# Kernel optimization log

Measured on AMD Instinct MI355X. Metric: run time of the kernel, lower is better.

## Reference

```python
import jax, jax.numpy as jnp
import numpy as np

D_IN = 1024
D_OUT = 1024
NUM_HEADS = 16
HEAD_DIM = D_OUT // NUM_HEADS


def setup_inputs() -> dict:
    key = jax.random.key(0)
    ks = jax.random.split(key, 7)
    s = 0.02
    x = jax.random.normal(ks[0], (2, 2048, D_IN), dtype=jnp.float32)
    # torch nn.Linear stores weight as [out, in]; y = x @ W.T + b
    w_k = jax.random.normal(ks[1], (D_OUT, D_IN), dtype=jnp.float32) * s
    w_q = jax.random.normal(ks[2], (D_OUT, D_IN), dtype=jnp.float32) * s
    w_v = jax.random.normal(ks[3], (D_OUT, D_IN), dtype=jnp.float32) * s
    w_o = jax.random.normal(ks[4], (D_OUT, D_OUT), dtype=jnp.float32) * s
    b_o = jax.random.normal(ks[5], (D_OUT,), dtype=jnp.float32) * s
    return {"x": x, "w_k": w_k, "w_q": w_q, "w_v": w_v, "w_o": w_o, "b_o": b_o}


def reference(x, w_k, w_q, w_v, w_o, b_o):
    b, L, _ = x.shape
    # NOTE (faithful to source): queries are produced by k_w, keys by q_w
    q = jnp.einsum('bld,od->blo', x, w_k)  # weighted_q = k_w(x)
    k = jnp.einsum('bld,od->blo', x, w_q)  # weighted_k = q_w(x)
    v = jnp.einsum('bld,od->blo', x, w_v)
    # [b, H, L, hd]
    q = q.reshape(b, L, NUM_HEADS, HEAD_DIM).transpose(0, 2, 1, 3)
    k = k.reshape(b, L, NUM_HEADS, HEAD_DIM).transpose(0, 2, 1, 3)
    v = v.reshape(b, L, NUM_HEADS, HEAD_DIM).transpose(0, 2, 1, 3)
    scores = jnp.einsum('bhqd,bhkd->bhqk', q, k)  # [b,H,L,L]
    causal = jnp.triu(jnp.ones((L, L), dtype=bool), k=1)  # True above diagonal
    scores = jnp.where(causal[None, None], -jnp.inf, scores)
    scale = jnp.float32(1.0 / np.sqrt(D_OUT))  # source scales by 1/sqrt(d_out)
    attn = jax.nn.softmax(scores * scale, axis=-1)
    ctx = jnp.einsum('bhqk,bhkd->bhqd', attn, v)
    ctx = ctx.transpose(0, 2, 1, 3).reshape(b, L, D_OUT)
    return jnp.einsum('blo,po->blp', ctx, w_o) + b_o
```

## Files before the change

### kernel.cpp

```cpp
#include <hip/hip_runtime.h>
#include <hip/hip_bf16.h>


typedef __attribute__((ext_vector_type(8))) short bf16x8;
typedef __attribute__((ext_vector_type(4))) float f32x4;

#define SEQ 2048
#define NHEAD 16
#define HD 64
#define M_TOT 4096

static __device__ __forceinline__ unsigned short f2bf(float f) {
  unsigned int u = __float_as_uint(f);
  u += 0x7fff + ((u >> 16) & 1);
  return (unsigned short)(u >> 16);
}
static __device__ __forceinline__ float bf2f(unsigned short u) {
  return __uint_as_float(((unsigned int)u) << 16);
}
static __device__ __forceinline__ unsigned int cvt_pk_bf16(float lo, float hi) {
  unsigned int r;
  asm("v_cvt_pk_bf16_f32 %0, %1, %2" : "=v"(r) : "v"(lo), "v"(hi));
  return r;
}

static __device__ __forceinline__ void gload16(const unsigned short* g, unsigned short* l) {
  __builtin_amdgcn_global_load_lds(
      (const __attribute__((address_space(1))) unsigned int*)g,
      (__attribute__((address_space(3))) unsigned int*)l, 16, 0, 0);
}

__global__ void cvt_kernel(const float* __restrict__ in, unsigned short* __restrict__ out, int n) {
  int i = (blockIdx.x * blockDim.x + threadIdx.x) * 4;
  if (i >= n) return;
  float4 v = *reinterpret_cast<const float4*>(in + i);
  ushort4 o;
  o.x = f2bf(v.x); o.y = f2bf(v.y); o.z = f2bf(v.z); o.w = f2bf(v.w);
  *reinterpret_cast<ushort4*>(out + i) = o;
}

__global__ void cvt4_kernel(const float* __restrict__ w0, const float* __restrict__ w1,
                            const float* __restrict__ w2, const float* __restrict__ w3,
                            unsigned short* __restrict__ o0, unsigned short* __restrict__ o1,
                            unsigned short* __restrict__ o2, unsigned short* __restrict__ o3) {
  const float* in; unsigned short* out;
  switch (blockIdx.y) {
    case 0: in = w0; out = o0; break;
    case 1: in = w1; out = o1; break;
    case 2: in = w2; out = o2; break;
    default: in = w3; out = o3; break;
  }
  int i = (blockIdx.x * blockDim.x + threadIdx.x) * 4;
  float4 v = *reinterpret_cast<const float4*>(in + i);
  ushort4 o;
  o.x = f2bf(v.x); o.y = f2bf(v.y); o.z = f2bf(v.z); o.w = f2bf(v.w);
  *reinterpret_cast<ushort4*>(out + i) = o;
}

template <int BN, int MODE>
__global__ __launch_bounds__(256) void gemm_tile(
    const unsigned short* __restrict__ A,
    const unsigned short* __restrict__ B,
    int K,
    unsigned short* __restrict__ qb,
    unsigned short* __restrict__ kb,
    unsigned short* __restrict__ vtb,
    const float* __restrict__ bias,
    float* __restrict__ outf)
{
  constexpr int NFR = BN / 32;
  __shared__ unsigned short lds_a[128 * 64];
  __shared__ unsigned short lds_b[BN * 64];
  const int t = threadIdx.x;
  const int wid = t >> 6;
  const int lane = t & 63;
  const int lr = lane & 15;
  const int lg = lane >> 4;
  const int tm = blockIdx.x * 128;
  const int tn = blockIdx.y * BN;
  const int wr = (wid >> 1) * 64;
  const int wc = (wid & 1) * (BN / 2);

  const unsigned short* Ab = A + (size_t)tm * K;
  const unsigned short* Bb = B + (size_t)tn * K;
  const int srow = wid * 8 + (lane >> 3);
  const int scol = (lane & 7) * 8;

  f32x4 acc[4][NFR];
  #pragma unroll
  for (int i = 0; i < 4; ++i)
    #pragma unroll
    for (int j = 0; j < NFR; ++j) acc[i][j] = (f32x4){0.f, 0.f, 0.f, 0.f};

  for (int k0 = 0; k0 < K; k0 += 64) {
    #pragma unroll
    for (int i = 0; i < 4; ++i)
      gload16(Ab + (size_t)(i * 32 + srow) * K + k0 + scol, &lds_a[(i * 32 + wid * 8) * 64]);
    #pragma unroll
    for (int i = 0; i < NFR; ++i)
      gload16(Bb + (size_t)(i * 32 + srow) * K + k0 + scol, &lds_b[(i * 32 + wid * 8) * 64]);
    __syncthreads();
    #pragma unroll
    for (int kk = 0; kk < 2; ++kk) {
      bf16x8 af[4], bfr[NFR];
      #pragma unroll
      for (int mi = 0; mi < 4; ++mi)
        af[mi] = *reinterpret_cast<const bf16x8*>(&lds_a[(wr + mi * 16 + lr) * 64 + kk * 32 + lg * 8]);
      #pragma unroll
      for (int ni = 0; ni < NFR; ++ni)
        bfr[ni] = *reinterpret_cast<const bf16x8*>(&lds_b[(wc + ni * 16 + lr) * 64 + kk * 32 + lg * 8]);
      #pragma unroll
      for (int mi = 0; mi < 4; ++mi)
        #pragma unroll
        for (int ni = 0; ni < NFR; ++ni)
          acc[mi][ni] = __builtin_amdgcn_mfma_f32_16x16x32_bf16(af[mi], bfr[ni], acc[mi][ni], 0, 0, 0);
    }
    __syncthreads();
  }

  if (MODE == 0) {
    #pragma unroll
    for (int mi = 0; mi < 4; ++mi)
      #pragma unroll
      for (int ni = 0; ni < NFR; ++ni)
        #pragma unroll
        for (int r = 0; r < 4; ++r) {
          int gm = tm + wr + mi * 16 + lg * 4 + r;
          int gn = tn + wc + ni * 16 + lr;
          float v = acc[mi][ni][r];
          unsigned short bv = f2bf(v);
          int bb = gm >> 11, l = gm & 2047;
          int tsel = gn >> 10, o = gn & 1023;
          int h = o >> 6, d = o & 63;
          if (tsel == 0)      qb[(((size_t)(bb * NHEAD + h)) * SEQ + l) * HD + d] = bv;
          else if (tsel == 1) kb[(((size_t)(bb * NHEAD + h)) * SEQ + l) * HD + d] = bv;
          else                vtb[(((size_t)(bb * NHEAD + h)) * HD + d) * SEQ + l] = bv;
        }
  } else {
    #pragma unroll
    for (int mi = 0; mi < 4; ++mi)
      #pragma unroll
      for (int ni = 0; ni < NFR; ++ni)
        #pragma unroll
        for (int r = 0; r < 4; ++r) {
          int gm = tm + wr + mi * 16 + lg * 4 + r;
          int gn = tn + wc + ni * 16 + lr;
          outf[(size_t)gm * 1024 + gn] = acc[mi][ni][r] + bias[gn];
        }
  }
}

__global__ __launch_bounds__(256) void attn_kernel(
    const unsigned short* __restrict__ qb,
    const unsigned short* __restrict__ kb,
    const unsigned short* __restrict__ vtb,
    unsigned short* __restrict__ ctxb)
{
  __shared__ unsigned short kt_lds[2][64 * 64];
  __shared__ unsigned short vt_lds[2][64 * 64];
  __shared__ unsigned short p_lds[4][16 * 64];

  const int t = threadIdx.x;
  const int wid = t >> 6;
  const int lane = t & 63;
  const int lr = lane & 15;
  const int lg = lane >> 4;

  const int id = blockIdx.x;
  const int xcd = id & 7;
  const int chunk = id >> 3;
  const int bh = xcd * 4 + (chunk >> 4);
  const int pair = chunk & 15;
  const int b = bh >> 4, h = bh & 15;

  const float csc = (1.0f / 32.0f) * 1.44269504f;

  const unsigned short* Kp = kb + (size_t)bh * SEQ * HD;
  const unsigned short* Vp = vtb + (size_t)bh * HD * SEQ;
  const int sr_ = lane >> 3;
  const int sg_ = lane & 7;

  auto stage = [&](int buf, int kv0) {
    #pragma unroll
    for (int i = 0; i < 2; ++i) {
      int r = i * 32 + wid * 8 + sr_;
      int g = sg_ ^ (r & 7);
      gload16(Kp + (size_t)(kv0 + r) * HD + g * 8, &kt_lds[buf][(i * 32 + wid * 8) * 64]);
      gload16(Vp + (size_t)r * SEQ + kv0 + g * 8, &vt_lds[buf][(i * 32 + wid * 8) * 64]);
    }
  };

  for (int ph = 0; ph < 2; ++ph) {
    const int qtile = ph ? pair : (31 - pair);
    const int qw = qtile * 64 + wid * 16;

    const unsigned short* Qp = qb + ((size_t)bh * SEQ + qw) * HD;
    bf16x8 aq[2];
    #pragma unroll
    for (int kk = 0; kk < 2; ++kk) {
      bf16x8 raw = *reinterpret_cast<const bf16x8*>(&Qp[lr * HD + kk * 32 + lg * 8]);
      #pragma unroll
      for (int j = 0; j < 8; ++j)
        aq[kk][j] = (short)f2bf(bf2f((unsigned short)raw[j]) * csc);
    }

    f32x4 oacc[4];
    #pragma unroll
    for (int ni = 0; ni < 4; ++ni) oacc[ni] = (f32x4){0.f, 0.f, 0.f, 0.f};
    float m_ = -INFINITY, ls = 0.f;

    stage(0, 0);
    __syncthreads();
    int cur = 0;

    for (int kt = 0; kt <= qtile; ++kt) {
      const int kv0 = kt * 64;
      if (kt < qtile) stage(cur ^ 1, kv0 + 64);

      const char* kbase = (const char*)&kt_lds[cur][0];
      f32x4 s4[4];
      #pragma unroll
      for (int ni = 0; ni < 4; ++ni) {
        int row = ni * 16 + lr;
        int xr = (row & 7) << 4;
        bf16x8 b0 = *reinterpret_cast<const bf16x8*>(kbase + (row * 128 + ((lg * 16) ^ xr)));
        bf16x8 b1 = *reinterpret_cast<const bf16x8*>(kbase + (row * 128 + ((64 + lg * 16) ^ xr)));
        s4[ni] = (f32x4){0.f, 0.f, 0.f, 0.f};
        s4[ni] = __builtin_amdgcn_mfma_f32_16x16x32_bf16(b0, aq[0], s4[ni], 0, 0, 0);
        s4[ni] = __builtin_amdgcn_mfma_f32_16x16x32_bf16(b1, aq[1], s4[ni], 0, 0, 0);
      }

      if (kt == qtile) {
        #pragma unroll
        for (int ni = 0; ni < 4; ++ni)
          #pragma unroll
          for (int r = 0; r < 4; ++r)
            if (ni * 16 + lg * 4 + r > wid * 16 + lr) s4[ni][r] = -INFINITY;
      }

      float rmax;
      {
        float a0 = fmaxf(fmaxf(s4[0][0], s4[0][1]), fmaxf(s4[0][2], s4[0][3]));
        float a1 = fmaxf(fmaxf(s4[1][0], s4[1][1]), fmaxf(s4[1][2], s4[1][3]));
        float a2 = fmaxf(fmaxf(s4[2][0], s4[2][1]), fmaxf(s4[2][2], s4[2][3]));
        float a3 = fmaxf(fmaxf(s4[3][0], s4[3][1]), fmaxf(s4[3][2], s4[3][3]));
        rmax = fmaxf(fmaxf(a0, a1), fmaxf(a2, a3));
        rmax = fmaxf(rmax, __shfl_xor(rmax, 16));
        rmax = fmaxf(rmax, __shfl_xor(rmax, 32));
      }

      if (__any(rmax > m_ + 8.f)) {
        float mn = fmaxf(m_, rmax);
        float f = exp2f(m_ - mn);
        m_ = mn;
        ls *= f;
        #pragma unroll
        for (int r = 0; r < 4; ++r) {
          float fo = __shfl(f, lg * 4 + r);
          #pragma unroll
          for (int ni = 0; ni < 4; ++ni) oacc[ni][r] *= fo;
        }
      }

      float p[4][4];
      float psum = 0.f;
      #pragma unroll
      for (int ni = 0; ni < 4; ++ni) {
        float t0 = exp2f(s4[ni][0] - m_);
        float t1 = exp2f(s4[ni][1] - m_);
        float t2 = exp2f(s4[ni][2] - m_);
        float t3 = exp2f(s4[ni][3] - m_);
        p[ni][0] = t0; p[ni][1] = t1; p[ni][2] = t2; p[ni][3] = t3;
        psum += (t0 + t1) + (t2 + t3);
      }
      psum += __shfl_xor(psum, 16);
      psum += __shfl_xor(psum, 32);
      ls += psum;

      char* pbase = (char*)&p_lds[wid][0];
      const int xq = (lr & 7) << 4;
      #pragma unroll
      for (int ni = 0; ni < 4; ++ni) {
        uint2 w;
        w.x = cvt_pk_bf16(p[ni][0], p[ni][1]);
        w.y = cvt_pk_bf16(p[ni][2], p[ni][3]);
        *reinterpret_cast<uint2*>(pbase + ((lr * 128 + ni * 32 + lg * 8) ^ xq)) = w;
      }

      bf16x8 pa0 = *reinterpret_cast<const bf16x8*>(pbase + ((lr * 128 + lg * 16) ^ xq));
      bf16x8 pa1 = *reinterpret_cast<const bf16x8*>(pbase + ((lr * 128 + 64 + lg * 16) ^ xq));

      const char* vbase = (const char*)&vt_lds[cur][0];
      #pragma unroll
      for (int ni = 0; ni < 4; ++ni) {
        int row = ni * 16 + lr;
        int xr = (row & 7) << 4;
        bf16x8 v0 = *reinterpret_cast<const bf16x8*>(vbase + (row * 128 + ((lg * 16) ^ xr)));
        bf16x8 v1 = *reinterpret_cast<const bf16x8*>(vbase + (row * 128 + ((64 + lg * 16) ^ xr)));
        oacc[ni] = __builtin_amdgcn_mfma_f32_16x16x32_bf16(pa0, v0, oacc[ni], 0, 0, 0);
        oacc[ni] = __builtin_amdgcn_mfma_f32_16x16x32_bf16(pa1, v1, oacc[ni], 0, 0, 0);
      }

      __syncthreads();
      cur ^= 1;
    }

    #pragma unroll
    for (int r = 0; r < 4; ++r) {
      float inv = 1.0f / __shfl(ls, lg * 4 + r);
      int qr = qw + lg * 4 + r;
      #pragma unroll
      for (int ni = 0; ni < 4; ++ni) {
        int d = ni * 16 + lr;
        ctxb[((size_t)b * SEQ + qr) * 1024 + h * HD + d] = f2bf(oacc[ni][r] * inv);
      }
    }
  }
}

extern "C" void kernel_launch(void* const* d_in, const int* in_sizes, int n_in,
                              void* d_out, int out_size, void* d_ws, size_t ws_size,
                              hipStream_t stream) {
  const float* x   = (const float*)d_in[0];
  const float* w_k = (const float*)d_in[1];
  const float* w_q = (const float*)d_in[2];
  const float* w_v = (const float*)d_in[3];
  const float* w_o = (const float*)d_in[4];
  const float* b_o = (const float*)d_in[5];
  float* out = (float*)d_out;

  char* ws = (char*)d_ws;
  unsigned short* xb   = (unsigned short*)(ws + 0);
  unsigned short* wqkv = (unsigned short*)(ws + 8388608);
  unsigned short* wob  = (unsigned short*)(ws + 14680064);
  unsigned short* qb   = (unsigned short*)(ws + 16777216);
  unsigned short* kb   = (unsigned short*)(ws + 25165824);
  unsigned short* vtb  = (unsigned short*)(ws + 33554432);
  unsigned short* ctxb = xb;

  int n = M_TOT * 1024;
  cvt_kernel<<<n / 1024, 256, 0, stream>>>(x, xb, n);
  cvt4_kernel<<<dim3(1024, 4), 256, 0, stream>>>(
      w_k, w_q, w_v, w_o, wqkv, wqkv + 1048576, wqkv + 2097152, wob);

  gemm_tile<96, 0><<<dim3(32, 32), 256, 0, stream>>>(
      xb, wqkv, 1024, qb, kb, vtb, nullptr, nullptr);

  attn_kernel<<<dim3(512), 256, 0, stream>>>(qb, kb, vtb, ctxb);

  gemm_tile<64, 1><<<dim3(32, 16), 256, 0, stream>>>(
      ctxb, wob, 1024, nullptr, nullptr, nullptr, b_o, out);
}
```

Baseline: 217.3 us.

## Double-buffer GEMM LDS tiles and XOR-swizzle rows to avoid bank conflicts

The projection GEMM kernel now keeps two LDS buffers per operand and issues the global-to-LDS loads for the next K-step before computing on the current one. This lets memory latency overlap with MFMA work and removes one barrier per iteration. The global column chunk for each row is also XOR-swizzled by the row index, so LDS fragment reads in the MFMA loop avoid bank conflicts. In exchange, LDS use doubles, which may lower occupancy.

```diff
diff --git a/kernel.cpp b/kernel.cpp
--- a/kernel.cpp
+++ b/kernel.cpp
@@ -69,8 +69,8 @@
     float* __restrict__ outf)
 {
   constexpr int NFR = BN / 32;
-  __shared__ unsigned short lds_a[128 * 64];
-  __shared__ unsigned short lds_b[BN * 64];
+  __shared__ unsigned short lds_a[2][128 * 64];
+  __shared__ unsigned short lds_b[2][BN * 64];
   const int t = threadIdx.x;
   const int wid = t >> 6;
   const int lane = t & 63;
@@ -83,8 +83,25 @@
 
   const unsigned short* Ab = A + (size_t)tm * K;
   const unsigned short* Bb = B + (size_t)tn * K;
-  const int srow = wid * 8 + (lane >> 3);
-  const int scol = (lane & 7) * 8;
+  const int sr_ = lane >> 3;
+  const int sg_ = lane & 7;
+
+  auto stageA = [&](int buf, int k0) {
+    #pragma unroll
+    for (int i = 0; i < 4; ++i) {
+      int r = i * 32 + wid * 8 + sr_;
+      int g = sg_ ^ (r & 7);
+      gload16(Ab + (size_t)r * K + k0 + g * 8, &lds_a[buf][(i * 32 + wid * 8) * 64]);
+    }
+  };
+  auto stageB = [&](int buf, int k0) {
+    #pragma unroll
+    for (int i = 0; i < NFR; ++i) {
+      int r = i * 32 + wid * 8 + sr_;
+      int g = sg_ ^ (r & 7);
+      gload16(Bb + (size_t)r * K + k0 + g * 8, &lds_b[buf][(i * 32 + wid * 8) * 64]);
+    }
+  };
 
   f32x4 acc[4][NFR];
   #pragma unroll
@@ -92,23 +109,33 @@
     #pragma unroll
     for (int j = 0; j < NFR; ++j) acc[i][j] = (f32x4){0.f, 0.f, 0.f, 0.f};
 
-  for (int k0 = 0; k0 < K; k0 += 64) {
-    #pragma unroll
-    for (int i = 0; i < 4; ++i)
-      gload16(Ab + (size_t)(i * 32 + srow) * K + k0 + scol, &lds_a[(i * 32 + wid * 8) * 64]);
-    #pragma unroll
-    for (int i = 0; i < NFR; ++i)
-      gload16(Bb + (size_t)(i * 32 + srow) * K + k0 + scol, &lds_b[(i * 32 + wid * 8) * 64]);
-    __syncthreads();
+  stageA(0, 0); stageB(0, 0);
+  __syncthreads();
+  int cur = 0;
+  const int nks = K >> 6;
+
+  for (int ks = 0; ks < nks; ++ks) {
+    if (ks + 1 < nks) {
+      stageA(cur ^ 1, (ks + 1) * 64);
+      stageB(cur ^ 1, (ks + 1) * 64);
+    }
+    const char* abase = (const char*)&lds_a[cur][0];
+    const char* bbase = (const char*)&lds_b[cur][0];
     #pragma unroll
     for (int kk = 0; kk < 2; ++kk) {
       bf16x8 af[4], bfr[NFR];
       #pragma unroll
-      for (int mi = 0; mi < 4; ++mi)
-        af[mi] = *reinterpret_cast<const bf16x8*>(&lds_a[(wr + mi * 16 + lr) * 64 + kk * 32 + lg * 8]);
-      #pragma unroll
-      for (int ni = 0; ni < NFR; ++ni)
-        bfr[ni] = *reinterpret_cast<const bf16x8*>(&lds_b[(wc + ni * 16 + lr) * 64 + kk * 32 + lg * 8]);
+      for (int mi = 0; mi < 4; ++mi) {
+        int row = wr + mi * 16 + lr;
+        af[mi] = *reinterpret_cast<const bf16x8*>(
+            abase + row * 128 + ((kk * 64 + lg * 16) ^ ((row & 7) << 4)));
+      }
+      #pragma unroll
+      for (int ni = 0; ni < NFR; ++ni) {
+        int row = wc + ni * 16 + lr;
+        bfr[ni] = *reinterpret_cast<const bf16x8*>(
+            bbase + row * 128 + ((kk * 64 + lg * 16) ^ ((row & 7) << 4)));
+      }
       #pragma unroll
       for (int mi = 0; mi < 4; ++mi)
         #pragma unroll
@@ -116,6 +143,7 @@
           acc[mi][ni] = __builtin_amdgcn_mfma_f32_16x16x32_bf16(af[mi], bfr[ni], acc[mi][ni], 0, 0, 0);
     }
     __syncthreads();
+    cur ^= 1;
   }
 
   if (MODE == 0) {
```

Result: faster. 201.0 us (-7.5%).
